# Kernel optimization log

Measured on AMD Instinct MI355X. Metric: run time of the kernel, lower is better.

## Reference

```python
import jax, jax.numpy as jnp
import numpy as np

FOCAL_LEVEL = 3
KERNEL_SIZES = [3, 5, 7]  # focal_factor*k + focal_window for k in 0..2
EPS = 1e-5


def _ln(x, g, b):
    mu = jnp.mean(x, axis=-1, keepdims=True)
    var = jnp.mean(jnp.square(x - mu), axis=-1, keepdims=True)
    return (x - mu) * jax.lax.rsqrt(var + EPS) * g + b


def _gelu(x):
    return jax.nn.gelu(x, approximate=False)


def _dwconv(x, k):
    # x: [B,H,W,C], k: [kh,kw,1,C] depthwise kernel
    return jax.lax.conv_general_dilated(
        x, k, window_strides=(1, 1), padding='SAME',
        dimension_numbers=('NHWC', 'HWIO', 'NHWC'),
        feature_group_count=x.shape[-1])


def setup_inputs() -> dict:
    key = jax.random.key(0)
    B, H, W, C = 64, 56, 56, 128
    hidden = 4 * C
    ks = jax.random.split(key, 16)
    s = 0.02
    inp = {
        'x': jax.random.normal(ks[0], (B, H * W, C), jnp.float32),
        'f_w': jax.random.normal(ks[1], (C, 2 * C + FOCAL_LEVEL + 1), jnp.float32) * s,
        'f_b': jnp.zeros((2 * C + FOCAL_LEVEL + 1,), jnp.float32),
        'k0': jax.random.normal(ks[2], (3, 3, 1, C), jnp.float32) * s,
        'k1': jax.random.normal(ks[3], (5, 5, 1, C), jnp.float32) * s,
        'k2': jax.random.normal(ks[4], (7, 7, 1, C), jnp.float32) * s,
        'h_w': jax.random.normal(ks[5], (C, C), jnp.float32) * s,
        'h_b': jnp.zeros((C,), jnp.float32),
        'proj_w': jax.random.normal(ks[6], (C, C), jnp.float32) * s,
        'proj_b': jnp.zeros((C,), jnp.float32),
        'ln1_g': jnp.ones((C,), jnp.float32),
        'ln1_b': jnp.zeros((C,), jnp.float32),
        'ln2_g': jnp.ones((C,), jnp.float32),
        'ln2_b': jnp.zeros((C,), jnp.float32),
        'fc1_w': jax.random.normal(ks[7], (C, hidden), jnp.float32) * s,
        'fc1_b': jnp.zeros((hidden,), jnp.float32),
        'fc2_w': jax.random.normal(ks[8], (hidden, C), jnp.float32) * s,
        'fc2_b': jnp.zeros((C,), jnp.float32),
        'H': H,
        'W': W,
    }
    return inp


def reference(x, f_w, f_b, k0, k1, k2, h_w, h_b, proj_w, proj_b,
              ln1_g, ln1_b, ln2_g, ln2_b, fc1_w, fc1_b, fc2_w, fc2_b, H, W):
    B, L, C = x.shape
    shortcut = x
    y = _ln(x, ln1_g, ln1_b).reshape(B, H, W, C)

    # --- FocalModulation ---
    t = y @ f_w + f_b  # [B,H,W,2C+fl+1]
    q = t[..., :C]
    ctx = t[..., C:2 * C]
    gates = t[..., 2 * C:]
    kernels = [k0, k1, k2]
    ctx_all = jnp.zeros_like(ctx)
    for l in range(FOCAL_LEVEL):
        ctx = _gelu(_dwconv(ctx, kernels[l]))
        ctx_all = ctx_all + ctx * gates[..., l:l + 1]
    ctx_global = _gelu(jnp.mean(ctx, axis=(1, 2), keepdims=True))  # GAP of last-level ctx
    ctx_all = ctx_all + ctx_global * gates[..., FOCAL_LEVEL:]
    modulator = ctx_all @ h_w + h_b  # 1x1 conv == channel matmul
    x_out = q * modulator
    x_out = x_out @ proj_w + proj_b
    x_out = x_out.reshape(B, H * W, C)

    x1 = shortcut + x_out
    # --- MLP branch ---
    m = _ln(x1, ln2_g, ln2_b)
    m = _gelu(m @ fc1_w + fc1_b) @ fc2_w + fc2_b
    return x1 + m
```

## Files before the change

### kernel.cpp

```cpp
#include <hip/hip_runtime.h>
#include <hip/hip_bf16.h>


#define NT 200704
#define CC 128
#define HH 56
#define WW 56
#define BB 64

typedef short short8 __attribute__((ext_vector_type(8)));
typedef float f32x4  __attribute__((ext_vector_type(4)));

__device__ __forceinline__ float b2f(unsigned short u) {
    union { float f; unsigned int i; } v; v.i = ((unsigned int)u) << 16; return v.f;
}
__device__ __forceinline__ unsigned short f2b(float f) {
    __hip_bfloat16 h = __float2bfloat16(f);
    union { __hip_bfloat16 h; unsigned short u; } v; v.h = h; return v.u;
}
__device__ __forceinline__ float gelu(float x) {
    float x2 = x * x;
    float inner = fmaf(0.044715f * x2, x, x);
    float t = exp2f(inner * -2.302118070f);
    return x * __builtin_amdgcn_rcpf(1.0f + t);
}
__device__ __forceinline__ void cvt4(uint2 p, float* o) {
    union { float f; unsigned int i; } v;
    v.i = p.x << 16;         o[0] = v.f;
    v.i = p.x & 0xffff0000u; o[1] = v.f;
    v.i = p.y << 16;         o[2] = v.f;
    v.i = p.y & 0xffff0000u; o[3] = v.f;
}
__device__ __forceinline__ void cvt2(unsigned int p, float* o) {
    union { float f; unsigned int i; } v;
    v.i = p << 16;          o[0] = v.f;
    v.i = p & 0xffff0000u;  o[1] = v.f;
}
__device__ __forceinline__ unsigned int pack2(float a, float b) {
    return (unsigned int)f2b(a) | ((unsigned int)f2b(b) << 16);
}
__device__ __forceinline__ uint2 pack4(const float* s) {
    uint2 r;
    r.x = (unsigned int)f2b(s[0]) | ((unsigned int)f2b(s[1]) << 16);
    r.y = (unsigned int)f2b(s[2]) | ((unsigned int)f2b(s[3]) << 16);
    return r;
}
__device__ __forceinline__ short8 ldfrag_g(const unsigned short* p) {
    union { uint4 u; short8 s; } v;
    v.u = *(const uint4*)p;
    return v.s;
}
__device__ __forceinline__ short8 ldfrag_s(const unsigned short* p) {
    return *(const short8*)p;
}

__global__ void transpose_bf16_k(const float* __restrict__ src, unsigned short* __restrict__ dst,
                                 int K, int M, int src_ld) {
    int idx = blockIdx.x * 256 + threadIdx.x;
    if (idx >= K * M) return;
    int k = idx / M, m = idx - k * M;
    dst[m * K + k] = f2b(src[k * src_ld + m]);
}
__global__ void transpose_fc2c_k(const float* __restrict__ src, unsigned short* __restrict__ dst) {
    int idx = blockIdx.x * 256 + threadIdx.x;
    if (idx >= 512 * 128) return;
    int k = idx >> 7, m = idx & 127;
    int hc = k >> 7, kl = k & 127;
    dst[hc * 16384 + m * 128 + kl] = f2b(src[k * 128 + m]);
}

__global__ __launch_bounds__(256) void ln1_gates_k(
    const float* __restrict__ x, const float* __restrict__ g, const float* __restrict__ bta,
    const float* __restrict__ fw, const float* __restrict__ fb,
    unsigned short* __restrict__ ybf, float* __restrict__ gates)
{
    int lane = threadIdx.x & 63, wv = threadIdx.x >> 6;
    int token = blockIdx.x * 4 + wv;
    float2 xv = *(const float2*)&x[(size_t)token * CC + lane * 2];
    float s = xv.x + xv.y;
    for (int o = 32; o; o >>= 1) s += __shfl_xor(s, o);
    float mu = s * (1.0f / 128.0f);
    float d0 = xv.x - mu, d1 = xv.y - mu;
    float q2 = d0 * d0 + d1 * d1;
    for (int o = 32; o; o >>= 1) q2 += __shfl_xor(q2, o);
    float rs = rsqrtf(q2 * (1.0f / 128.0f) + 1e-5f);
    float y0 = d0 * rs * g[2 * lane] + bta[2 * lane];
    float y1 = d1 * rs * g[2 * lane + 1] + bta[2 * lane + 1];
    unsigned int pk = (unsigned int)f2b(y0) | ((unsigned int)f2b(y1) << 16);
    ((unsigned int*)ybf)[(size_t)token * 64 + lane] = pk;
    float ga[4];
    #pragma unroll
    for (int gg = 0; gg < 4; gg++)
        ga[gg] = y0 * fw[(2 * lane) * 260 + 256 + gg] + y1 * fw[(2 * lane + 1) * 260 + 256 + gg];
    for (int o = 32; o; o >>= 1) {
        #pragma unroll
        for (int gg = 0; gg < 4; gg++) ga[gg] += __shfl_xor(ga[gg], o);
    }
    if (lane == 0) {
        float4 gv = make_float4(ga[0] + fb[256], ga[1] + fb[257], ga[2] + fb[258], ga[3] + fb[259]);
        *(float4*)&gates[(size_t)token * 4] = gv;
    }
}

__global__ __launch_bounds__(256) void ln2_k(
    const float* __restrict__ x, const float* __restrict__ g, const float* __restrict__ bta,
    unsigned short* __restrict__ ybf)
{
    int lane = threadIdx.x & 63, wv = threadIdx.x >> 6;
    int token = blockIdx.x * 4 + wv;
    float2 xv = *(const float2*)&x[(size_t)token * CC + lane * 2];
    float s = xv.x + xv.y;
    for (int o = 32; o; o >>= 1) s += __shfl_xor(s, o);
    float mu = s * (1.0f / 128.0f);
    float d0 = xv.x - mu, d1 = xv.y - mu;
    float q2 = d0 * d0 + d1 * d1;
    for (int o = 32; o; o >>= 1) q2 += __shfl_xor(q2, o);
    float rs = rsqrtf(q2 * (1.0f / 128.0f) + 1e-5f);
    float y0 = d0 * rs * g[2 * lane] + bta[2 * lane];
    float y1 = d1 * rs * g[2 * lane + 1] + bta[2 * lane + 1];
    unsigned int pk = (unsigned int)f2b(y0) | ((unsigned int)f2b(y1) << 16);
    ((unsigned int*)ybf)[(size_t)token * 64 + lane] = pk;
}


#define GEMM_IDS \
    const int row0 = blockIdx.x * 128; \
    const int lane = threadIdx.x & 63, wv = threadIdx.x >> 6; \
    const int wy = wv >> 1, wx = wv & 1; \
    const int q4 = lane >> 4, l16 = lane & 15; (void)row0;

#define ZERO_ACC(acc) \
    _Pragma("unroll") for (int i = 0; i < 4; i++) \
    _Pragma("unroll") for (int j = 0; j < 4; j++) acc[i][j] = (f32x4)0.0f;

#define MFMA_ALL(acc, af, bf) \
    _Pragma("unroll") for (int i = 0; i < 4; i++) \
    _Pragma("unroll") for (int j = 0; j < 4; j++) \
        acc[i][j] = __builtin_amdgcn_mfma_f32_16x16x32_bf16(af[i], bf[j], acc[i][j], 0, 0, 0);

#define STAGE_A(As, gsrc) \
    _Pragma("unroll") for (int it = 0; it < 8; it++) { \
        int idx = it * 256 + threadIdx.x; \
        int arow = idx >> 4, c16 = idx & 15; \
        *(uint4*)&As[arow * 136 + c16 * 8] = *(const uint4*)&(gsrc)[idx * 8]; \
    }

__global__ __launch_bounds__(256) void gemm_f2_k(
    const unsigned short* __restrict__ A, const unsigned short* __restrict__ Wt,
    const float* __restrict__ fb,
    unsigned short* __restrict__ outq, unsigned short* __restrict__ outcT)
{
    __shared__ unsigned short As[128 * 136];
    __shared__ unsigned short Gs[32 * 268];
    GEMM_IDS;
    STAGE_A(As, &A[(size_t)row0 * 128]);
    __syncthreads();
    #pragma unroll 1
    for (int mo = 0; mo < 2; mo++) {
        f32x4 acc[4][4];
        ZERO_ACC(acc);
        #pragma unroll
        for (int kk = 0; kk < 128; kk += 32) {
            short8 af[4], bf[4];
            #pragma unroll
            for (int i = 0; i < 4; i++)
                af[i] = ldfrag_s(&As[(wy * 64 + i * 16 + l16) * 136 + kk + q4 * 8]);
            #pragma unroll
            for (int j = 0; j < 4; j++)
                bf[j] = ldfrag_g(&Wt[(size_t)(mo * 128 + wx * 64 + j * 16 + l16) * 128 + kk + q4 * 8]);
            MFMA_ALL(acc, af, bf);
        }
        if (mo == 0) {
            #pragma unroll
            for (int i = 0; i < 4; i++)
                #pragma unroll
                for (int j = 0; j < 4; j++)
                    #pragma unroll
                    for (int rr = 0; rr < 4; rr++) {
                        int row = row0 + wy * 64 + i * 16 + q4 * 4 + rr;
                        int col = wx * 64 + j * 16 + l16;
                        outq[(size_t)row * CC + col] = f2b(acc[i][j][rr] + fb[col]);
                    }
        } else {
            #pragma unroll
            for (int i = 0; i < 4; i++)
                #pragma unroll
                for (int j = 0; j < 4; j++)
                    #pragma unroll
                    for (int rr = 0; rr < 4; rr++) {
                        int row_l = wy * 64 + i * 16 + q4 * 4 + rr;
                        int col = wx * 64 + j * 16 + l16;
                        Gs[(col >> 2) * 268 + row_l * 4 + (col & 3)] = f2b(acc[i][j][rr] + fb[128 + col]);
                    }
            __syncthreads();
            #pragma unroll
            for (int it = 0; it < 16; it++) {
                int c = it * 256 + threadIdx.x;
                int s = c >> 7, tok = c & 127;
                *(uint2*)&outcT[((size_t)s * NT + row0 + tok) * 4] =
                    *(const uint2*)&Gs[s * 268 + tok * 4];
            }
        }
    }
}

__global__ __launch_bounds__(256) void gemm_hproj_k(
    const unsigned short* __restrict__ CA, const unsigned short* __restrict__ Wh,
    const float* __restrict__ hb, const unsigned short* __restrict__ Qm,
    const unsigned short* __restrict__ Wp, const float* __restrict__ pb,
    const float* __restrict__ xin, float* __restrict__ outp)
{
    __shared__ unsigned short As2[32 * 128 * 4];
    __shared__ unsigned short Gs[128 * 136];
    GEMM_IDS;
    #pragma unroll
    for (int it = 0; it < 8; it++) {
        int idx = it * 256 + threadIdx.x;
        int s = idx >> 6, c = idx & 63;
        *(uint4*)&As2[(s * 128 + c * 2) * 4] =
            *(const uint4*)&CA[((size_t)s * NT + row0 + c * 2) * 4];
    }
    __syncthreads();
    f32x4 acc[4][4];
    ZERO_ACC(acc);
    #pragma unroll
    for (int kk = 0; kk < 128; kk += 32) {
        short8 af[4], bf[4];
        int s0 = (kk >> 2) + q4 * 2;
        #pragma unroll
        for (int i = 0; i < 4; i++) {
            int row_l = wy * 64 + i * 16 + l16;
            union { uint2 u[2]; short8 s; } v;
            v.u[0] = *(const uint2*)&As2[(s0 * 128 + row_l) * 4];
            v.u[1] = *(const uint2*)&As2[((s0 + 1) * 128 + row_l) * 4];
            af[i] = v.s;
        }
        #pragma unroll
        for (int j = 0; j < 4; j++)
            bf[j] = ldfrag_g(&Wh[(size_t)(wx * 64 + j * 16 + l16) * 128 + kk + q4 * 8]);
        MFMA_ALL(acc, af, bf);
    }
    #pragma unroll
    for (int i = 0; i < 4; i++)
        #pragma unroll
        for (int j = 0; j < 4; j++)
            #pragma unroll
            for (int rr = 0; rr < 4; rr++) {
                int row_l = wy * 64 + i * 16 + q4 * 4 + rr;
                int col_l = wx * 64 + j * 16 + l16;
                float v = acc[i][j][rr] + hb[col_l];
                float qv = b2f(Qm[(size_t)(row0 + row_l) * CC + col_l]);
                Gs[row_l * 136 + col_l] = f2b(v * qv);
            }
    __syncthreads();
    ZERO_ACC(acc);
    #pragma unroll
    for (int kk = 0; kk < 128; kk += 32) {
        short8 af[4], bf[4];
        #pragma unroll
        for (int i = 0; i < 4; i++)
            af[i] = ldfrag_s(&Gs[(wy * 64 + i * 16 + l16) * 136 + kk + q4 * 8]);
        #pragma unroll
        for (int j = 0; j < 4; j++)
            bf[j] = ldfrag_g(&Wp[(size_t)(wx * 64 + j * 16 + l16) * 128 + kk + q4 * 8]);
        MFMA_ALL(acc, af, bf);
    }
    #pragma unroll
    for (int i = 0; i < 4; i++)
        #pragma unroll
        for (int j = 0; j < 4; j++)
            #pragma unroll
            for (int rr = 0; rr < 4; rr++) {
                int row = row0 + wy * 64 + i * 16 + q4 * 4 + rr;
                int col = wx * 64 + j * 16 + l16;
                size_t oi = (size_t)row * CC + col;
                outp[oi] = acc[i][j][rr] + pb[col] + xin[oi];
            }
}

__global__ __launch_bounds__(256) void gemm_mlp_k(
    const unsigned short* __restrict__ M, const unsigned short* __restrict__ W1,
    const float* __restrict__ b1, const unsigned short* __restrict__ W2,
    const float* __restrict__ b2, float* __restrict__ outp)
{
    __shared__ unsigned short As[128 * 136];
    __shared__ unsigned short Gs[128 * 136];
    GEMM_IDS;
    STAGE_A(As, &M[(size_t)row0 * 128]);
    __syncthreads();
    f32x4 accO[4][4];
    ZERO_ACC(accO);
    #pragma unroll 1
    for (int hc = 0; hc < 4; hc++) {
        f32x4 accG[4][4];
        ZERO_ACC(accG);
        #pragma unroll
        for (int kk = 0; kk < 128; kk += 32) {
            short8 af[4], bf[4];
            #pragma unroll
            for (int i = 0; i < 4; i++)
                af[i] = ldfrag_s(&As[(wy * 64 + i * 16 + l16) * 136 + kk + q4 * 8]);
            #pragma unroll
            for (int j = 0; j < 4; j++)
                bf[j] = ldfrag_g(&W1[(size_t)(hc * 128 + wx * 64 + j * 16 + l16) * 128 + kk + q4 * 8]);
            MFMA_ALL(accG, af, bf);
        }
        __syncthreads();
        #pragma unroll
        for (int i = 0; i < 4; i++)
            #pragma unroll
            for (int j = 0; j < 4; j++)
                #pragma unroll
                for (int rr = 0; rr < 4; rr++) {
                    int row_l = wy * 64 + i * 16 + q4 * 4 + rr;
                    int col_l = wx * 64 + j * 16 + l16;
                    Gs[row_l * 136 + col_l] = f2b(gelu(accG[i][j][rr] + b1[hc * 128 + col_l]));
                }
        __syncthreads();
        #pragma unroll
        for (int kk = 0; kk < 128; kk += 32) {
            short8 af[4], bf[4];
            #pragma unroll
            for (int i = 0; i < 4; i++)
                af[i] = ldfrag_s(&Gs[(wy * 64 + i * 16 + l16) * 136 + kk + q4 * 8]);
            #pragma unroll
            for (int j = 0; j < 4; j++)
                bf[j] = ldfrag_g(&W2[(size_t)hc * 16384 + (wx * 64 + j * 16 + l16) * 128 + kk + q4 * 8]);
            MFMA_ALL(accO, af, bf);
        }
    }
    #pragma unroll
    for (int i = 0; i < 4; i++)
        #pragma unroll
        for (int j = 0; j < 4; j++)
            #pragma unroll
            for (int rr = 0; rr < 4; rr++) {
                int row = row0 + wy * 64 + i * 16 + q4 * 4 + rr;
                int col = wx * 64 + j * 16 + l16;
                size_t oi = (size_t)row * CC + col;
                outp[oi] = accO[i][j][rr] + b2[col] + outp[oi];
            }
}

template<int R, bool SUM>
__device__ __forceinline__ void conv_half(
    const unsigned int* __restrict__ bin, unsigned int* __restrict__ bout,
    const float2* __restrict__ wl2h, int t0, const float* __restrict__ gates,
    int r, int w0, int tok0, int level, float creg[7][2], float psum[2])
{
    constexpr int KS = 2 * R + 1;
    float acc7[7][2];
    #pragma unroll
    for (int i = 0; i < 7; i++) { acc7[i][0] = 0.0f; acc7[i][1] = 0.0f; }
    #pragma unroll
    for (int kh = 0; kh < KS; kh++) {
        const unsigned int* rp = &bin[(r + kh + 3 - R) * 65 + (w0 + 3 - R)];
        float xw[7 + 2 * R][2];
        #pragma unroll
        for (int j = 0; j < 7 + 2 * R; j++) cvt2(rp[j], xw[j]);
        #pragma unroll
        for (int kw = 0; kw < KS; kw++) {
            float2 w2 = wl2h[(t0 + kh * KS + kw) * 2];
            #pragma unroll
            for (int ow = 0; ow < 7; ow++) {
                acc7[ow][0] += xw[ow + kw][0] * w2.x;
                acc7[ow][1] += xw[ow + kw][1] * w2.y;
            }
        }
    }
    #pragma unroll
    for (int ow = 0; ow < 7; ow++) {
        float gt = gates[(size_t)(tok0 + ow) * 4 + level];
        float g0 = gelu(acc7[ow][0]);
        float g1 = gelu(acc7[ow][1]);
        creg[ow][0] += g0 * gt;
        creg[ow][1] += g1 * gt;
        if (SUM) { psum[0] += g0; psum[1] += g1; }
        if (!SUM) bout[(r + 3) * 65 + (w0 + 3 + ow)] = pack2(g0, g1);
    }
}

__global__ __launch_bounds__(448) void dwconv_fused_k(
    const unsigned short* __restrict__ cinT,
    const float* __restrict__ k0w, const float* __restrict__ k1w, const float* __restrict__ k2w,
    const float* __restrict__ gates,
    unsigned short* __restrict__ coutT, float* __restrict__ part)
{
    constexpr int PL = 62 * 65;
    __shared__ unsigned int bufA[2][PL];
    __shared__ unsigned int bufB[2][PL];
    __shared__ float2 wl2[83 * 2];
    __shared__ float wred[7][4];
    const int tid = threadIdx.x;
    const int slab = blockIdx.x, b = blockIdx.y;

    for (int i = tid; i < PL; i += 448) {
        bufA[0][i] = 0u; bufA[1][i] = 0u;
        bufB[0][i] = 0u; bufB[1][i] = 0u;
    }
    if (tid < 166) {
        int t = tid >> 1, h = tid & 1;
        const float* src = (t < 9) ? &k0w[t * CC]
                         : (t < 34) ? &k1w[(t - 9) * CC]
                                    : &k2w[(t - 34) * CC];
        wl2[t * 2 + h] = *(const float2*)&src[slab * 4 + h * 2];
    }
    __syncthreads();
    const unsigned short* cinS = cinT + ((size_t)slab * BB + b) * 3136 * 4;
    for (int px = tid; px < 3136; px += 448) {
        int rr = px / 56, c = px - rr * 56;
        uint2 v = *(const uint2*)&cinS[(size_t)px * 4];
        bufA[0][(rr + 3) * 65 + c + 3] = v.x;
        bufA[1][(rr + 3) * 65 + c + 3] = v.y;
    }
    __syncthreads();

    const int r = tid >> 3, wt = tid & 7, w0 = wt * 7;
    const int tok0 = b * 3136 + r * 56 + w0;
    float creg[2][7][2];
    #pragma unroll
    for (int h = 0; h < 2; h++)
        #pragma unroll
        for (int i = 0; i < 7; i++) { creg[h][i][0] = 0.0f; creg[h][i][1] = 0.0f; }
    float psum[4] = {0.0f, 0.0f, 0.0f, 0.0f};

    #pragma unroll
    for (int h = 0; h < 2; h++) {
        conv_half<1, false>(bufA[h], bufB[h], wl2 + h, 0,  gates, r, w0, tok0, 0, creg[h], &psum[h * 2]);
        __syncthreads();
        conv_half<2, false>(bufB[h], bufA[h], wl2 + h, 9,  gates, r, w0, tok0, 1, creg[h], &psum[h * 2]);
        __syncthreads();
        conv_half<3, true >(bufA[h], bufB[h], wl2 + h, 34, gates, r, w0, tok0, 2, creg[h], &psum[h * 2]);
    }

    unsigned short* coutS = coutT + ((size_t)slab * BB + b) * 3136 * 4;
    #pragma unroll
    for (int ow = 0; ow < 7; ow++) {
        float s4[4] = {creg[0][ow][0], creg[0][ow][1], creg[1][ow][0], creg[1][ow][1]};
        *(uint2*)&coutS[(size_t)(r * 56 + w0 + ow) * 4] = pack4(s4);
    }

    #pragma unroll
    for (int e = 0; e < 4; e++)
        for (int o = 32; o; o >>= 1) psum[e] += __shfl_xor(psum[e], o);
    if ((tid & 63) == 0) {
        #pragma unroll
        for (int e = 0; e < 4; e++) wred[tid >> 6][e] = psum[e];
    }
    __syncthreads();
    if (tid == 0) {
        float s0 = 0, s1 = 0, s2 = 0, s3 = 0;
        for (int w2 = 0; w2 < 7; w2++) {
            s0 += wred[w2][0]; s1 += wred[w2][1]; s2 += wred[w2][2]; s3 += wred[w2][3];
        }
        float4 res = make_float4(s0, s1, s2, s3);
        *(float4*)&part[((size_t)b * 32 + slab) * 4] = res;
    }
}

__global__ void mean_fin_k(const float* __restrict__ part, float* __restrict__ cg) {
    int b = blockIdx.x, c = threadIdx.x;
    cg[b * CC + c] = gelu(part[b * CC + c] * (1.0f / 3136.0f));
}

__global__ __launch_bounds__(256) void addg3_k(
    unsigned short* acc, const float* __restrict__ gates, const float* __restrict__ cg)
{
    unsigned int idx4 = blockIdx.x * 256 + threadIdx.x;
    unsigned int s   = idx4 / NT;
    unsigned int tok = idx4 - s * NT;
    unsigned int b   = tok / 3136;
    float g3 = gates[(size_t)tok * 4 + 3];
    const float* cgp = &cg[b * CC + s * 4];
    uint2 v = *(uint2*)&acc[(size_t)idx4 * 4];
    float f[4];
    cvt4(v, f);
    #pragma unroll
    for (int e = 0; e < 4; e++) f[e] += cgp[e] * g3;
    *(uint2*)&acc[(size_t)idx4 * 4] = pack4(f);
}

extern "C" void kernel_launch(void* const* d_in, const int* in_sizes, int n_in,
                              void* d_out, int out_size, void* d_ws, size_t ws_size,
                              hipStream_t stream) {
    (void)in_sizes; (void)n_in; (void)out_size; (void)ws_size;
    const float* x      = (const float*)d_in[0];
    const float* f_w    = (const float*)d_in[1];
    const float* f_b    = (const float*)d_in[2];
    const float* k0     = (const float*)d_in[3];
    const float* k1     = (const float*)d_in[4];
    const float* k2     = (const float*)d_in[5];
    const float* h_w    = (const float*)d_in[6];
    const float* h_b    = (const float*)d_in[7];
    const float* proj_w = (const float*)d_in[8];
    const float* proj_b = (const float*)d_in[9];
    const float* ln1_g  = (const float*)d_in[10];
    const float* ln1_b  = (const float*)d_in[11];
    const float* ln2_g  = (const float*)d_in[12];
    const float* ln2_b  = (const float*)d_in[13];
    const float* fc1_w  = (const float*)d_in[14];
    const float* fc1_b  = (const float*)d_in[15];
    const float* fc2_w  = (const float*)d_in[16];
    const float* fc2_b  = (const float*)d_in[17];
    float* out = (float*)d_out;

    size_t off = 0;
    auto alloc = [&](size_t bytes) -> char* {
        char* p = (char*)d_ws + off;
        off += (bytes + 255) & ~(size_t)255;
        return p;
    };
    unsigned short* wt_f    = (unsigned short*)alloc(256 * 128 * 2);
    unsigned short* wt_h    = (unsigned short*)alloc(128 * 128 * 2);
    unsigned short* wt_proj = (unsigned short*)alloc(128 * 128 * 2);
    unsigned short* wt_fc1  = (unsigned short*)alloc(512 * 128 * 2);
    unsigned short* wt_fc2c = (unsigned short*)alloc(512 * 128 * 2);
    unsigned short* Y       = (unsigned short*)alloc((size_t)NT * CC * 2);
    unsigned short* Q       = (unsigned short*)alloc((size_t)NT * CC * 2);
    float*          gates   = (float*)alloc((size_t)NT * 4 * 4);
    float*          part    = (float*)alloc(BB * CC * 4);
    float*          cg      = (float*)alloc(BB * CC * 4);

    unsigned short* p1 = (unsigned short*)d_out + (size_t)NT * CC;

    transpose_bf16_k<<<(128 * 256 + 255) / 256, 256, 0, stream>>>(f_w, wt_f, 128, 256, 260);
    transpose_bf16_k<<<(128 * 128 + 255) / 256, 256, 0, stream>>>(h_w, wt_h, 128, 128, 128);
    transpose_bf16_k<<<(128 * 128 + 255) / 256, 256, 0, stream>>>(proj_w, wt_proj, 128, 128, 128);
    transpose_bf16_k<<<(128 * 512 + 255) / 256, 256, 0, stream>>>(fc1_w, wt_fc1, 128, 512, 512);
    transpose_fc2c_k<<<(512 * 128 + 255) / 256, 256, 0, stream>>>(fc2_w, wt_fc2c);

    ln1_gates_k<<<NT / 4, 256, 0, stream>>>(x, ln1_g, ln1_b, f_w, f_b, Y, gates);

    gemm_f2_k<<<NT / 128, 256, 0, stream>>>(Y, wt_f, f_b, Q, p1);

    dwconv_fused_k<<<dim3(32, BB), 448, 0, stream>>>(p1, k0, k1, k2, gates, Y, part);

    mean_fin_k<<<BB, 128, 0, stream>>>(part, cg);
    addg3_k<<<NT * 32 / 256, 256, 0, stream>>>(Y, gates, cg);

    gemm_hproj_k<<<NT / 128, 256, 0, stream>>>(Y, wt_h, h_b, Q, wt_proj, proj_b, x, out);

    ln2_k<<<NT / 4, 256, 0, stream>>>(out, ln2_g, ln2_b, Y);

    gemm_mlp_k<<<NT / 128, 256, 0, stream>>>(Y, wt_fc1, fc1_b, wt_fc2c, fc2_b, out);
}
```

Measured before the change: 929.7 us.

## Fuse LayerNorm1 into focal GEMM and LayerNorm2 into proj GEMM epilogue

```diff
diff --git a/kernel.cpp b/kernel.cpp
--- a/kernel.cpp
+++ b/kernel.cpp
@@ -69,59 +69,6 @@
     dst[hc * 16384 + m * 128 + kl] = f2b(src[k * 128 + m]);
 }
 
-__global__ __launch_bounds__(256) void ln1_gates_k(
-    const float* __restrict__ x, const float* __restrict__ g, const float* __restrict__ bta,
-    const float* __restrict__ fw, const float* __restrict__ fb,
-    unsigned short* __restrict__ ybf, float* __restrict__ gates)
-{
-    int lane = threadIdx.x & 63, wv = threadIdx.x >> 6;
-    int token = blockIdx.x * 4 + wv;
-    float2 xv = *(const float2*)&x[(size_t)token * CC + lane * 2];
-    float s = xv.x + xv.y;
-    for (int o = 32; o; o >>= 1) s += __shfl_xor(s, o);
-    float mu = s * (1.0f / 128.0f);
-    float d0 = xv.x - mu, d1 = xv.y - mu;
-    float q2 = d0 * d0 + d1 * d1;
-    for (int o = 32; o; o >>= 1) q2 += __shfl_xor(q2, o);
-    float rs = rsqrtf(q2 * (1.0f / 128.0f) + 1e-5f);
-    float y0 = d0 * rs * g[2 * lane] + bta[2 * lane];
-    float y1 = d1 * rs * g[2 * lane + 1] + bta[2 * lane + 1];
-    unsigned int pk = (unsigned int)f2b(y0) | ((unsigned int)f2b(y1) << 16);
-    ((unsigned int*)ybf)[(size_t)token * 64 + lane] = pk;
-    float ga[4];
-    #pragma unroll
-    for (int gg = 0; gg < 4; gg++)
-        ga[gg] = y0 * fw[(2 * lane) * 260 + 256 + gg] + y1 * fw[(2 * lane + 1) * 260 + 256 + gg];
-    for (int o = 32; o; o >>= 1) {
-        #pragma unroll
-        for (int gg = 0; gg < 4; gg++) ga[gg] += __shfl_xor(ga[gg], o);
-    }
-    if (lane == 0) {
-        float4 gv = make_float4(ga[0] + fb[256], ga[1] + fb[257], ga[2] + fb[258], ga[3] + fb[259]);
-        *(float4*)&gates[(size_t)token * 4] = gv;
-    }
-}
-
-__global__ __launch_bounds__(256) void ln2_k(
-    const float* __restrict__ x, const float* __restrict__ g, const float* __restrict__ bta,
-    unsigned short* __restrict__ ybf)
-{
-    int lane = threadIdx.x & 63, wv = threadIdx.x >> 6;
-    int token = blockIdx.x * 4 + wv;
-    float2 xv = *(const float2*)&x[(size_t)token * CC + lane * 2];
-    float s = xv.x + xv.y;
-    for (int o = 32; o; o >>= 1) s += __shfl_xor(s, o);
-    float mu = s * (1.0f / 128.0f);
-    float d0 = xv.x - mu, d1 = xv.y - mu;
-    float q2 = d0 * d0 + d1 * d1;
-    for (int o = 32; o; o >>= 1) q2 += __shfl_xor(q2, o);
-    float rs = rsqrtf(q2 * (1.0f / 128.0f) + 1e-5f);
-    float y0 = d0 * rs * g[2 * lane] + bta[2 * lane];
-    float y1 = d1 * rs * g[2 * lane + 1] + bta[2 * lane + 1];
-    unsigned int pk = (unsigned int)f2b(y0) | ((unsigned int)f2b(y1) << 16);
-    ((unsigned int*)ybf)[(size_t)token * 64 + lane] = pk;
-}
-
 
 #define GEMM_IDS \
     const int row0 = blockIdx.x * 128; \
@@ -146,15 +93,55 @@
     }
 
 __global__ __launch_bounds__(256) void gemm_f2_k(
-    const unsigned short* __restrict__ A, const unsigned short* __restrict__ Wt,
-    const float* __restrict__ fb,
-    unsigned short* __restrict__ outq, unsigned short* __restrict__ outcT)
+    const float* __restrict__ x, const float* __restrict__ g1, const float* __restrict__ b1,
+    const float* __restrict__ fw, const float* __restrict__ fb,
+    const unsigned short* __restrict__ Wt,
+    unsigned short* __restrict__ outq, unsigned short* __restrict__ outcT,
+    float* __restrict__ gates)
 {
     __shared__ unsigned short As[128 * 136];
     __shared__ unsigned short Gs[32 * 268];
     GEMM_IDS;
-    STAGE_A(As, &A[(size_t)row0 * 128]);
-    __syncthreads();
+
+    {
+        float gch0 = g1[2 * lane], gch1 = g1[2 * lane + 1];
+        float bch0 = b1[2 * lane], bch1 = b1[2 * lane + 1];
+        float fw0[4], fw1[4];
+        #pragma unroll
+        for (int gg = 0; gg < 4; gg++) {
+            fw0[gg] = fw[(2 * lane) * 260 + 256 + gg];
+            fw1[gg] = fw[(2 * lane + 1) * 260 + 256 + gg];
+        }
+        for (int rr = 0; rr < 32; rr++) {
+            int row_l = wv * 32 + rr;
+            int token = row0 + row_l;
+            float2 xv = *(const float2*)&x[(size_t)token * CC + lane * 2];
+            float s = xv.x + xv.y;
+            for (int o = 32; o; o >>= 1) s += __shfl_xor(s, o);
+            float mu = s * (1.0f / 128.0f);
+            float d0 = xv.x - mu, d1 = xv.y - mu;
+            float q2 = d0 * d0 + d1 * d1;
+            for (int o = 32; o; o >>= 1) q2 += __shfl_xor(q2, o);
+            float rs = rsqrtf(q2 * (1.0f / 128.0f) + 1e-5f);
+            float y0 = d0 * rs * gch0 + bch0;
+            float y1 = d1 * rs * gch1 + bch1;
+            ((unsigned int*)As)[row_l * 68 + lane] = pack2(y0, y1);
+            float ga[4];
+            #pragma unroll
+            for (int gg = 0; gg < 4; gg++) ga[gg] = y0 * fw0[gg] + y1 * fw1[gg];
+            for (int o = 32; o; o >>= 1) {
+                #pragma unroll
+                for (int gg = 0; gg < 4; gg++) ga[gg] += __shfl_xor(ga[gg], o);
+            }
+            if (lane == 0) {
+                float4 gv = make_float4(ga[0] + fb[256], ga[1] + fb[257],
+                                        ga[2] + fb[258], ga[3] + fb[259]);
+                *(float4*)&gates[(size_t)token * 4] = gv;
+            }
+        }
+    }
+    __syncthreads();
+
     #pragma unroll 1
     for (int mo = 0; mo < 2; mo++) {
         f32x4 acc[4][4];
@@ -208,7 +195,9 @@
     const unsigned short* __restrict__ CA, const unsigned short* __restrict__ Wh,
     const float* __restrict__ hb, const unsigned short* __restrict__ Qm,
     const unsigned short* __restrict__ Wp, const float* __restrict__ pb,
-    const float* __restrict__ xin, float* __restrict__ outp)
+    const float* __restrict__ xin, float* __restrict__ outp,
+    const float* __restrict__ g2, const float* __restrict__ b2,
+    unsigned short* __restrict__ mout)
 {
     __shared__ unsigned short As2[32 * 128 * 4];
     __shared__ unsigned short Gs[128 * 136];
@@ -265,17 +254,41 @@
             bf[j] = ldfrag_g(&Wp[(size_t)(wx * 64 + j * 16 + l16) * 128 + kk + q4 * 8]);
         MFMA_ALL(acc, af, bf);
     }
+    __syncthreads();
     #pragma unroll
     for (int i = 0; i < 4; i++)
         #pragma unroll
         for (int j = 0; j < 4; j++)
             #pragma unroll
             for (int rr = 0; rr < 4; rr++) {
-                int row = row0 + wy * 64 + i * 16 + q4 * 4 + rr;
+                int row_l = wy * 64 + i * 16 + q4 * 4 + rr;
                 int col = wx * 64 + j * 16 + l16;
-                size_t oi = (size_t)row * CC + col;
-                outp[oi] = acc[i][j][rr] + pb[col] + xin[oi];
-            }
+                size_t oi = (size_t)(row0 + row_l) * CC + col;
+                float v = acc[i][j][rr] + pb[col] + xin[oi];
+                outp[oi] = v;
+                Gs[row_l * 136 + col] = f2b(v);
+            }
+    __syncthreads();
+    {
+        float gch0 = g2[2 * lane], gch1 = g2[2 * lane + 1];
+        float bch0 = b2[2 * lane], bch1 = b2[2 * lane + 1];
+        for (int rr = 0; rr < 32; rr++) {
+            int row_l = wv * 32 + rr;
+            int token = row0 + row_l;
+            float xv[2];
+            cvt2(((const unsigned int*)Gs)[row_l * 68 + lane], xv);
+            float s = xv[0] + xv[1];
+            for (int o = 32; o; o >>= 1) s += __shfl_xor(s, o);
+            float mu = s * (1.0f / 128.0f);
+            float d0 = xv[0] - mu, d1 = xv[1] - mu;
+            float q2 = d0 * d0 + d1 * d1;
+            for (int o = 32; o; o >>= 1) q2 += __shfl_xor(q2, o);
+            float rs = rsqrtf(q2 * (1.0f / 128.0f) + 1e-5f);
+            float y0 = d0 * rs * gch0 + bch0;
+            float y1 = d1 * rs * gch1 + bch1;
+            ((unsigned int*)mout)[(size_t)token * 64 + lane] = pack2(y0, y1);
+        }
+    }
 }
 
 __global__ __launch_bounds__(256) void gemm_mlp_k(
@@ -529,18 +542,15 @@
     transpose_bf16_k<<<(128 * 512 + 255) / 256, 256, 0, stream>>>(fc1_w, wt_fc1, 128, 512, 512);
     transpose_fc2c_k<<<(512 * 128 + 255) / 256, 256, 0, stream>>>(fc2_w, wt_fc2c);
 
-    ln1_gates_k<<<NT / 4, 256, 0, stream>>>(x, ln1_g, ln1_b, f_w, f_b, Y, gates);
-
-    gemm_f2_k<<<NT / 128, 256, 0, stream>>>(Y, wt_f, f_b, Q, p1);
+    gemm_f2_k<<<NT / 128, 256, 0, stream>>>(x, ln1_g, ln1_b, f_w, f_b, wt_f, Q, p1, gates);
 
     dwconv_fused_k<<<dim3(32, BB), 448, 0, stream>>>(p1, k0, k1, k2, gates, Y, part);
 
     mean_fin_k<<<BB, 128, 0, stream>>>(part, cg);
     addg3_k<<<NT * 32 / 256, 256, 0, stream>>>(Y, gates, cg);
 
-    gemm_hproj_k<<<NT / 128, 256, 0, stream>>>(Y, wt_h, h_b, Q, wt_proj, proj_b, x, out);
-
-    ln2_k<<<NT / 4, 256, 0, stream>>>(out, ln2_g, ln2_b, Y);
-
-    gemm_mlp_k<<<NT / 128, 256, 0, stream>>>(Y, wt_fc1, fc1_b, wt_fc2c, fc2_b, out);
-}
+    gemm_hproj_k<<<NT / 128, 256, 0, stream>>>(Y, wt_h, h_b, Q, wt_proj, proj_b, x, out,
+                                               ln2_g, ln2_b, Q);
+
+    gemm_mlp_k<<<NT / 128, 256, 0, stream>>>(Q, wt_fc1, fc1_b, wt_fc2c, fc2_b, out);
+}
```

Result: slower. 1.016 ms (+9.3%).
